# Performance work log

Hardware: AMD Instinct MI355X
Metric: run time of the kernel (lower is better)

The kernel has to match this reference:

```python
import jax, jax.numpy as jnp
import numpy as np

N = 20000        # nodes
E = 640000       # edges (avg degree 32)
IN, H1, H2 = 512, 256, 128

def setup_inputs() -> dict:
    key = jax.random.key(0)
    k_feat, k_ew, k_src, k_dst, k_w1, k_w2 = jax.random.split(key, 6)
    return {
        "features": jax.random.normal(k_feat, (N, IN), jnp.float32),
        "edge_weight": jax.random.uniform(k_ew, (E,), jnp.float32),
        "src": jax.random.randint(k_src, (E,), 0, N),
        "dst": jax.random.randint(k_dst, (E,), 0, N),
        # learned params (GraphConv weight uses xavier-style init; bias zeros)
        "W1": jax.random.normal(k_w1, (IN, H1), jnp.float32) / np.float32(np.sqrt(IN)),
        "b1": jnp.zeros((H1,), jnp.float32),
        "W2": jax.random.normal(k_w2, (H1, H2), jnp.float32) / np.float32(np.sqrt(H1)),
        "b2": jnp.zeros((H2,), jnp.float32),
    }

def reference(features, edge_weight, src, dst, W1, b1, W2, b2):
    seg = lambda v, idx: jax.ops.segment_sum(v, idx, num_segments=N)

    # --- EdgeWeightNorm(norm='both'):
    # w_e / sqrt(out_wsum(src_e) * in_wsum(dst_e))
    out_wsum = seg(edge_weight, src)           # weighted out-degree  [N]
    in_wsum = seg(edge_weight, dst)            # weighted in-degree   [N]
    nw = edge_weight * jax.lax.rsqrt(out_wsum[src]) * jax.lax.rsqrt(in_wsum[dst])  # [E]

    # --- GraphConv layer 1: norm='none', edge_weight=nw, relu
    # in_feats > out_feats -> transform first, then weighted aggregation
    h = features @ W1                          # [N, H1]
    h = seg(h[src] * nw[:, None], dst) + b1    # SpMM: sum_e nw_e * h[src_e] at dst
    h = jax.nn.relu(h)

    # --- GraphConv layer 2: norm='both' (plain degrees, clamped min 1), identity act
    ones_e = jnp.ones((E,), h.dtype)
    out_deg = jnp.maximum(seg(ones_e, src), 1.0)   # out-degrees [N]
    in_deg = jnp.maximum(seg(ones_e, dst), 1.0)    # in-degrees  [N]
    h = h * jax.lax.rsqrt(out_deg)[:, None]        # src-side norm
    h = h @ W2                                     # [N, H2] (in > out -> W first)
    h = seg(h[src], dst)                           # unweighted sum aggregation
    h = h * jax.lax.rsqrt(in_deg)[:, None] + b2    # dst-side norm + bias
    return h
```

## Files before the change

### kernel.cpp

```cpp
#include <hip/hip_runtime.h>
#include <hip/hip_bf16.h>
#include <hip/hip_fp16.h>
#include <stdint.h>

#define IN_F 512
#define H1_F 256
#define H2_F 128
#define MPAD 20096
#define NN   20000
#define NPAIR 10000
#define BH   128
#define CAP  128
#define GB1  (157 * 2)

typedef __attribute__((ext_vector_type(8))) _Float16 half8;
typedef __attribute__((ext_vector_type(4))) float f32x4;
typedef __attribute__((ext_vector_type(4))) uint32_t u32x4;

__device__ inline __half2 h2cast(uint32_t v) { return __builtin_bit_cast(__half2, v); }
__device__ inline uint32_t h2bits(__half2 v) { return __builtin_bit_cast(uint32_t, v); }

__device__ inline void gld_lds16(const uint32_t* g, uint32_t* l) {
    __builtin_amdgcn_global_load_lds((const __attribute__((address_space(1))) uint32_t*)g,
                                     (__attribute__((address_space(3))) uint32_t*)l,
                                     16, 0, 0);
}

__device__ inline uint32_t packh2(float a, float b) {
    return (uint32_t)__builtin_bit_cast(unsigned short, (_Float16)a) |
           ((uint32_t)__builtin_bit_cast(unsigned short, (_Float16)b) << 16);
}

__global__ __launch_bounds__(512) void build_and_pack(
        const int* __restrict__ dst, const int* __restrict__ src,
        const float* __restrict__ ew,
        uint32_t* __restrict__ Pd, uint32_t* __restrict__ Ps, int E, int CH,
        const float* __restrict__ W1, const float* __restrict__ W2,
        uint16_t* __restrict__ Bt1, uint16_t* __restrict__ Bt2) {
    __shared__ uint32_t pd[NN];
    __shared__ uint32_t ps[NN];
    const int b = blockIdx.x, tid = threadIdx.x;
    if (b < BH) {
        for (int i = tid; i < NN; i += 512) { pd[i] = 0; ps[i] = 0; }
        __syncthreads();
        const int e0 = b * CH, e1 = min(e0 + CH, E);
        for (int e = e0 + tid; e < e1; e += 512) {
            uint32_t v = (1u << 24) | (uint32_t)__float2uint_rn(ew[e] * 65536.0f);
            atomicAdd(&pd[dst[e]], v);
            atomicAdd(&ps[src[e]], v);
        }
        __syncthreads();
        for (int i = tid; i < NN; i += 512) {
            Pd[(size_t)b * NN + i] = pd[i];
            Ps[(size_t)b * NN + i] = ps[i];
        }
    } else {
        const int pbid = b - BH;
        const int PBLK = gridDim.x - BH;
        const int stride = PBLK * 512;
        const int t1 = IN_F * H1_F;
        const int total = t1 + H1_F * H2_F;
        for (int i = pbid * 512 + tid; i < total; i += stride) {
            if (i < t1) {
                int k = i / H1_F, n = i - k * H1_F;
                Bt1[(size_t)n * IN_F + k] =
                    __builtin_bit_cast(unsigned short, (_Float16)W1[i]);
            } else {
                int i2 = i - t1;
                int k = i2 / H2_F, n = i2 - k * H2_F;
                Bt2[(size_t)n * H1_F + k] =
                    __builtin_bit_cast(unsigned short, (_Float16)W2[i2]);
            }
        }
    }
}

__global__ __launch_bounds__(256, 1) void gemm1_and_offsets(
        const float* __restrict__ A, const uint16_t* __restrict__ Bt,
        __half* __restrict__ Cout, int M, int K,
        const uint32_t* __restrict__ Pd, const uint32_t* __restrict__ Ps,
        uint16_t* __restrict__ Od,
        int* __restrict__ in_cnt, int* __restrict__ out_cnt,
        float* __restrict__ in_rs, float* __restrict__ out_rs, int N) {
    __shared__ uint32_t Al[128 * 16];
    __shared__ uint32_t Bl[128 * 16];
    const int bx = blockIdx.x;
    const int tid = threadIdx.x;
    if (bx >= GB1) {
        int i = (bx - GB1) * 256 + tid;
        if (i >= N) return;
        uint32_t cin = 0, cout = 0, win = 0, wout = 0;
        for (int b = 0; b < BH; ++b) {
            uint32_t vd = Pd[(size_t)b * NN + i];
            Od[(size_t)b * NN + i] = (uint16_t)cin;
            cin += vd >> 24; win += vd & 0xFFFFFFu;
            uint32_t vs = Ps[(size_t)b * NN + i];
            cout += vs >> 24; wout += vs & 0xFFFFFFu;
        }
        in_cnt[i] = (int)cin;
        out_cnt[i] = (int)cout;
        in_rs[i]  = cin  ? rsqrtf((float)win  * (1.0f / 65536.0f)) : 0.f;
        out_rs[i] = cout ? rsqrtf((float)wout * (1.0f / 65536.0f)) : 0.f;
        return;
    }
    const int xg = bx % 157, yg = bx / 157;
    const int lane = tid & 63, wid = tid >> 6;
    const int wm = wid >> 1, wn = wid & 1;
    const int l15 = lane & 15, lhi = lane >> 4;
    const int brow = xg * 128, bcol = yg * 128;

    f32x4 acc[4][4];
#pragma unroll
    for (int m = 0; m < 4; ++m)
#pragma unroll
        for (int n = 0; n < 4; ++n) acc[m][n] = f32x4{0.f, 0.f, 0.f, 0.f};

    for (int k0 = 0; k0 < K; k0 += 32) {
#pragma unroll
        for (int i = 0; i < 2; ++i) {
            int g = i * 256 + tid;
            int r = g >> 2, c16 = g & 3;
            int sA = (r & 3) ^ ((r >> 2) & 3);
            int c16s = c16 ^ sA;
            int gr = min(brow + r, M - 1);
            const float* gp = A + (size_t)gr * K + k0 + c16s * 8;
            float4 fa = *(const float4*)gp;
            float4 fb = *(const float4*)(gp + 4);
            u32x4 q;
            q.x = packh2(fa.x, fa.y);
            q.y = packh2(fa.z, fa.w);
            q.z = packh2(fb.x, fb.y);
            q.w = packh2(fb.z, fb.w);
            *(u32x4*)(Al + g * 4) = q;
        }
#pragma unroll
        for (int i = 0; i < 2; ++i) {
            int chunk = i * 256 + tid;
            int r = chunk >> 2, c16 = chunk & 3;
            int c16s = c16 ^ ((r & 3) ^ ((r >> 2) & 3));
            gld_lds16((const uint32_t*)(Bt + (size_t)(bcol + r) * K + k0) + c16s * 4,
                      Bl + chunk * 4);
        }
        __syncthreads();

        half8 am[4], bm[4];
#pragma unroll
        for (int m = 0; m < 4; ++m) {
            int row = wm * 64 + m * 16 + l15;
            int sA = (row & 3) ^ ((row >> 2) & 3);
            am[m] = __builtin_bit_cast(half8,
                        *(const u32x4*)(Al + row * 16 + ((lhi ^ sA) << 2)));
        }
#pragma unroll
        for (int n = 0; n < 4; ++n) {
            int col = wn * 64 + n * 16 + l15;
            int sB = (col & 3) ^ ((col >> 2) & 3);
            bm[n] = __builtin_bit_cast(half8,
                        *(const u32x4*)(Bl + col * 16 + ((lhi ^ sB) << 2)));
        }

#pragma unroll
        for (int m = 0; m < 4; ++m)
#pragma unroll
            for (int n = 0; n < 4; ++n)
                acc[m][n] = __builtin_amdgcn_mfma_f32_16x16x32_f16(am[m], bm[n],
                                                                   acc[m][n], 0, 0, 0);
        __syncthreads();
    }

#pragma unroll
    for (int m = 0; m < 4; ++m) {
        int rbase = brow + wm * 64 + m * 16 + lhi * 4;
#pragma unroll
        for (int n = 0; n < 4; ++n) {
            int col = bcol + wn * 64 + n * 16 + l15;
#pragma unroll
            for (int j = 0; j < 4; ++j) {
                int row = rbase + j;
                if (row < M)
                    Cout[(size_t)row * H1_F + col] = __float2half(acc[m][n][j]);
            }
        }
    }
}

__global__ __launch_bounds__(512) void scatter_dst(
        const int* __restrict__ src, const int* __restrict__ dst,
        const float* __restrict__ ew,
        const uint16_t* __restrict__ Od,
        const float* __restrict__ in_rs, const float* __restrict__ out_rs,
        unsigned long long* __restrict__ s_pk, int E, int CH) {
    __shared__ uint32_t h[NPAIR];
    const int b = blockIdx.x, tid = threadIdx.x;
    for (int i = tid; i < NPAIR; i += 512) h[i] = 0;
    __syncthreads();
    const int e0 = b * CH, e1 = min(e0 + CH, E);
    const uint16_t* Ob = Od + (size_t)b * NN;
    for (int e = e0 + tid; e < e1; e += 512) {
        int d = dst[e];
        uint32_t old = atomicAdd(&h[d >> 1], 1u << ((d & 1) * 16));
        uint32_t rank = (old >> ((d & 1) * 16)) & 0xffffu;
        int s = src[e];
        float nw = ew[e] * out_rs[s] * in_rs[d];
        int p = d * CAP + (int)Ob[d] + (int)rank;
        s_pk[p] = (unsigned long long)(unsigned)s |
                  ((unsigned long long)__builtin_bit_cast(unsigned, nw) << 32);
    }
}

__global__ __launch_bounds__(256, 1) void gemm2_f16(
        const uint16_t* __restrict__ At, const uint16_t* __restrict__ Bt,
        __half* __restrict__ Cout, const int* __restrict__ rowcnt,
        int M, int Nout, int K) {
    __shared__ uint32_t Al[128 * 16];
    __shared__ uint32_t Bl[128 * 16];
    const int tid = threadIdx.x;
    const int lane = tid & 63, wid = tid >> 6;
    const int wm = wid >> 1, wn = wid & 1;
    const int l15 = lane & 15, lhi = lane >> 4;
    const int brow = blockIdx.x * 128, bcol = blockIdx.y * 128;

    f32x4 acc[4][4];
#pragma unroll
    for (int m = 0; m < 4; ++m)
#pragma unroll
        for (int n = 0; n < 4; ++n) acc[m][n] = f32x4{0.f, 0.f, 0.f, 0.f};

    for (int k0 = 0; k0 < K; k0 += 32) {
#pragma unroll
        for (int i = 0; i < 2; ++i) {
            int chunk = i * 256 + tid;
            int r = chunk >> 2, c16 = chunk & 3;
            int c16s = c16 ^ ((r & 3) ^ ((r >> 2) & 3));
            gld_lds16((const uint32_t*)(At + (size_t)(brow + r) * K + k0) + c16s * 4,
                      Al + chunk * 4);
        }
#pragma unroll
        for (int i = 0; i < 2; ++i) {
            int chunk = i * 256 + tid;
            int r = chunk >> 2, c16 = chunk & 3;
            int c16s = c16 ^ ((r & 3) ^ ((r >> 2) & 3));
            gld_lds16((const uint32_t*)(Bt + (size_t)(bcol + r) * K + k0) + c16s * 4,
                      Bl + chunk * 4);
        }
        __syncthreads();

        half8 am[4], bm[4];
#pragma unroll
        for (int m = 0; m < 4; ++m) {
            int row = wm * 64 + m * 16 + l15;
            int sA = (row & 3) ^ ((row >> 2) & 3);
            am[m] = __builtin_bit_cast(half8,
                        *(const u32x4*)(Al + row * 16 + ((lhi ^ sA) << 2)));
        }
#pragma unroll
        for (int n = 0; n < 4; ++n) {
            int col = wn * 64 + n * 16 + l15;
            int sB = (col & 3) ^ ((col >> 2) & 3);
            bm[n] = __builtin_bit_cast(half8,
                        *(const u32x4*)(Bl + col * 16 + ((lhi ^ sB) << 2)));
        }

#pragma unroll
        for (int m = 0; m < 4; ++m)
#pragma unroll
            for (int n = 0; n < 4; ++n)
                acc[m][n] = __builtin_amdgcn_mfma_f32_16x16x32_f16(am[m], bm[n],
                                                                   acc[m][n], 0, 0, 0);
        __syncthreads();
    }

#pragma unroll
    for (int m = 0; m < 4; ++m) {
        int rbase = brow + wm * 64 + m * 16 + lhi * 4;
        float scl[4];
#pragma unroll
        for (int j = 0; j < 4; ++j) {
            scl[j] = 1.f;
            if (rbase + j < M)
                scl[j] = rsqrtf(fmaxf((float)rowcnt[rbase + j], 1.f));
        }
#pragma unroll
        for (int n = 0; n < 4; ++n) {
            int col = bcol + wn * 64 + n * 16 + l15;
#pragma unroll
            for (int j = 0; j < 4; ++j) {
                int row = rbase + j;
                if (row < M)
                    Cout[(size_t)row * Nout + col] = __float2half(acc[m][n][j] * scl[j]);
            }
        }
    }
}

__global__ void spmm1_h2(const uint4* __restrict__ h4,
                         const unsigned long long* __restrict__ s_pk,
                         const int* __restrict__ in_cnt,
                         const float* __restrict__ b1, uint16_t* __restrict__ h1f, int N) {
    int bx = blockIdx.x;
    int slice = bx & 3;
    int grp = bx >> 2;
    int wid = threadIdx.x >> 6, lane = threadIdx.x & 63;
    int node = grp * 4 + wid;
    if (node >= N) return;
    int start = node * CAP, cnt = in_cnt[node];
    int s_pre = 0; uint32_t w2_pre = 0;
    if (lane < cnt) {
        unsigned long long m = s_pk[start + lane];
        s_pre = (int)(unsigned)m;
        __half hw = __float2half(__builtin_bit_cast(float, (unsigned)(m >> 32)));
        w2_pre = h2bits(__halves2half2(hw, hw));
    }
    int el = lane >> 3, fo = lane & 7;
    const uint4* hb = h4 + slice * 8 + fo;
    __half2 acc[4];
#pragma unroll
    for (int k = 0; k < 4; ++k) acc[k] = h2cast(0u);
    int cnt1 = min(cnt, 64);
    int nb = (cnt1 + 7) >> 3;
    int s[8]; uint32_t w[8]; uint4 v[8];
#pragma unroll
    for (int g = 0; g < 8; ++g) {
        if (g < nb) {
            int j = el + g * 8;
            s[g] = __shfl(s_pre, j);
            w[g] = (uint32_t)__shfl((int)w2_pre, j);
            v[g] = hb[(size_t)s[g] * 32];
        }
    }
#pragma unroll
    for (int g = 0; g < 8; ++g) {
        if (g < nb) {
            __half2 wg = h2cast(w[g]);
            acc[0] = __hfma2(wg, h2cast(v[g].x), acc[0]);
            acc[1] = __hfma2(wg, h2cast(v[g].y), acc[1]);
            acc[2] = __hfma2(wg, h2cast(v[g].z), acc[2]);
            acc[3] = __hfma2(wg, h2cast(v[g].w), acc[3]);
        }
    }
    for (int j = 64 + el; j < cnt; j += 8) {
        unsigned long long m = s_pk[start + j];
        int sx = (int)(unsigned)m;
        __half hw = __float2half(__builtin_bit_cast(float, (unsigned)(m >> 32)));
        __half2 w2h = __halves2half2(hw, hw);
        uint4 vx = hb[(size_t)sx * 32];
        acc[0] = __hfma2(w2h, h2cast(vx.x), acc[0]);
        acc[1] = __hfma2(w2h, h2cast(vx.y), acc[1]);
        acc[2] = __hfma2(w2h, h2cast(vx.z), acc[2]);
        acc[3] = __hfma2(w2h, h2cast(vx.w), acc[3]);
    }
#pragma unroll
    for (int d = 8; d < 64; d <<= 1)
#pragma unroll
        for (int k = 0; k < 4; ++k) {
            uint32_t o = (uint32_t)__shfl_xor((int)h2bits(acc[k]), d);
            acc[k] = __hadd2(acc[k], h2cast(o));
        }
    if (el == 0) {
        int fi = slice * 64 + fo * 8;
        float2 f0 = __half22float2(acc[0]);
        float2 f1 = __half22float2(acc[1]);
        float2 f2 = __half22float2(acc[2]);
        float2 f3 = __half22float2(acc[3]);
        uint4 o;
        o.x = h2bits(__halves2half2(__float2half(fmaxf(f0.x + b1[fi + 0], 0.f)),
                                    __float2half(fmaxf(f0.y + b1[fi + 1], 0.f))));
        o.y = h2bits(__halves2half2(__float2half(fmaxf(f1.x + b1[fi + 2], 0.f)),
                                    __float2half(fmaxf(f1.y + b1[fi + 3], 0.f))));
        o.z = h2bits(__halves2half2(__float2half(fmaxf(f2.x + b1[fi + 4], 0.f)),
                                    __float2half(fmaxf(f2.y + b1[fi + 5], 0.f))));
        o.w = h2bits(__halves2half2(__float2half(fmaxf(f3.x + b1[fi + 6], 0.f)),
                                    __float2half(fmaxf(f3.y + b1[fi + 7], 0.f))));
        *(uint4*)(h1f + (size_t)node * H1_F + fi) = o;
    }
}

__global__ void spmm2_h2(const uint4* __restrict__ h4,
                         const unsigned long long* __restrict__ s_pk,
                         const int* __restrict__ in_cnt,
                         const float* __restrict__ b2, float* __restrict__ out, int N) {
    const uint32_t ONE2 = 0x3C003C00u;
    int bx = blockIdx.x;
    int slice = bx & 1;
    int grp = bx >> 1;
    int wid = threadIdx.x >> 6, lane = threadIdx.x & 63;
    int node = grp * 4 + wid;
    if (node >= N) return;
    int start = node * CAP, cnt = in_cnt[node];
    int s_pre = 0;
    if (lane < cnt) s_pre = (int)(unsigned)s_pk[start + lane];
    int el = lane >> 3, fo = lane & 7;
    const uint4* hb = h4 + slice * 8 + fo;
    __half2 acc0[4], acc1[4];
#pragma unroll
    for (int k = 0; k < 4; ++k) { acc0[k] = h2cast(0u); acc1[k] = h2cast(0u); }
    int cnt1 = min(cnt, 64);
    int nb = (cnt1 + 7) >> 3;
    int s[8]; __half2 w[8]; uint4 v[8];
#pragma unroll
    for (int g = 0; g < 8; ++g) {
        if (g < nb) {
            int j = el + g * 8;
            s[g] = __shfl(s_pre, j);
            w[g] = h2cast((j < cnt1) ? ONE2 : 0u);
            v[g] = hb[(size_t)s[g] * 16];
        }
    }
#pragma unroll
    for (int g = 0; g < 4; ++g) {
        if (g < nb) {
            acc0[0] = __hfma2(w[g], h2cast(v[g].x), acc0[0]);
            acc0[1] = __hfma2(w[g], h2cast(v[g].y), acc0[1]);
            acc0[2] = __hfma2(w[g], h2cast(v[g].z), acc0[2]);
            acc0[3] = __hfma2(w[g], h2cast(v[g].w), acc0[3]);
        }
    }
#pragma unroll
    for (int g = 4; g < 8; ++g) {
        if (g < nb) {
            acc1[0] = __hfma2(w[g], h2cast(v[g].x), acc1[0]);
            acc1[1] = __hfma2(w[g], h2cast(v[g].y), acc1[1]);
            acc1[2] = __hfma2(w[g], h2cast(v[g].z), acc1[2]);
            acc1[3] = __hfma2(w[g], h2cast(v[g].w), acc1[3]);
        }
    }
    for (int j = 64 + el; j < cnt; j += 8) {
        int sx = (int)(unsigned)s_pk[start + j];
        uint4 vx = hb[(size_t)sx * 16];
        __half2 one = h2cast(ONE2);
        acc0[0] = __hfma2(one, h2cast(vx.x), acc0[0]);
        acc0[1] = __hfma2(one, h2cast(vx.y), acc0[1]);
        acc0[2] = __hfma2(one, h2cast(vx.z), acc0[2]);
        acc0[3] = __hfma2(one, h2cast(vx.w), acc0[3]);
    }
    float accf[8];
#pragma unroll
    for (int k = 0; k < 4; ++k) {
        float2 a = __half22float2(acc0[k]);
        float2 b = __half22float2(acc1[k]);
        accf[2 * k]     = a.x + b.x;
        accf[2 * k + 1] = a.y + b.y;
    }
#pragma unroll
    for (int d = 8; d < 64; d <<= 1)
#pragma unroll
        for (int k = 0; k < 8; ++k) accf[k] += __shfl_xor(accf[k], d);
    if (el == 0) {
        float rin = rsqrtf(fmaxf((float)cnt, 1.f));
        int fi = slice * 64 + fo * 8;
        f32x4 r0, r1;
        r0.x = accf[0] * rin + b2[fi + 0];
        r0.y = accf[1] * rin + b2[fi + 1];
        r0.z = accf[2] * rin + b2[fi + 2];
        r0.w = accf[3] * rin + b2[fi + 3];
        r1.x = accf[4] * rin + b2[fi + 4];
        r1.y = accf[5] * rin + b2[fi + 5];
        r1.z = accf[6] * rin + b2[fi + 6];
        r1.w = accf[7] * rin + b2[fi + 7];
        float* dp = out + (size_t)node * H2_F + fi;
        *(f32x4*)dp = r0;
        *(f32x4*)(dp + 4) = r1;
    }
}

extern "C" void kernel_launch(void* const* d_in, const int* in_sizes, int n_in,
                              void* d_out, int out_size, void* d_ws, size_t ws_size,
                              hipStream_t stream) {
    const float* features = (const float*)d_in[0];
    const float* edge_w   = (const float*)d_in[1];
    const int*   src      = (const int*)d_in[2];
    const int*   dst      = (const int*)d_in[3];
    const float* W1       = (const float*)d_in[4];
    const float* b1       = (const float*)d_in[5];
    const float* W2       = (const float*)d_in[6];
    const float* b2       = (const float*)d_in[7];
    float* out = (float*)d_out;

    const int N = in_sizes[0] / IN_F;
    const int E = in_sizes[1];
    const int CH = (E + BH - 1) / BH;

    char* base = (char*)d_ws;
    size_t off = 0;
    auto alloc = [&](size_t bytes) {
        char* p = base + off;
        off = (off + bytes + 255) & ~(size_t)255;
        return p;
    };
    int*   out_cnt   = (int*)  alloc((size_t)N * 4);
    float* out_rs    = (float*)alloc((size_t)N * 4);
    int*   in_cnt    = (int*)  alloc((size_t)N * 4);
    float* in_rs     = (float*)alloc((size_t)N * 4);
    unsigned long long* s_pk = (unsigned long long*)alloc((size_t)NN * CAP * 8);
    uint16_t* Bt1    = (uint16_t*)alloc((size_t)H1_F * IN_F * 2);
    uint16_t* Bt2    = (uint16_t*)alloc((size_t)H2_F * H1_F * 2);
    __half* h_f16    = (__half*)alloc((size_t)MPAD * H1_F * 2);
    uint32_t* big    = (uint32_t*)alloc((size_t)BH * NN * 4 * 2 + (size_t)BH * NN * 2);
    uint32_t* Pd = big;
    uint32_t* Ps = big + (size_t)BH * NN;
    uint16_t* Od = (uint16_t*)(Ps + (size_t)BH * NN);
    uint16_t* h1f = (uint16_t*)big;
    __half*   h2f = (__half*)((uint16_t*)big + (size_t)MPAD * H1_F);
    (void)ws_size;

    build_and_pack<<<256, 512, 0, stream>>>(dst, src, edge_w, Pd, Ps, E, CH,
                                            W1, W2, Bt1, Bt2);

    int goBlocks = GB1 + (N + 255) / 256;
    gemm1_and_offsets<<<goBlocks, 256, 0, stream>>>(features, Bt1, h_f16, N, IN_F,
                                                    Pd, Ps, Od, in_cnt, out_cnt,
                                                    in_rs, out_rs, N);

    scatter_dst<<<BH, 512, 0, stream>>>(src, dst, edge_w, Od,
                                        in_rs, out_rs, s_pk, E, CH);

    int grp = (N + 3) / 4;
    spmm1_h2<<<grp * 4, 256, 0, stream>>>((const uint4*)h_f16, s_pk,
                                          in_cnt, b1, h1f, N);
    dim3 g2(MPAD / 128, 1);
    gemm2_f16<<<g2, 256, 0, stream>>>(h1f, Bt2, h2f, out_cnt, N, H2_F, H1_F);
    spmm2_h2<<<grp * 2, 256, 0, stream>>>((const uint4*)h2f, s_pk,
                                          in_cnt, b2, out, N);
}
```

Before: 122.7 us.

## Co-schedule GEMM1 with edge scatter and share A tile across column halves

The per-node offsets/rsqrt computation moves out of the GEMM1 launch into its own small kernel. The edge scatter then runs as extra blocks inside the GEMM1 launch instead of as a separate kernel. GEMM1 now uses 512-thread blocks, where each block converts one 128-row A tile to fp16 once and two 256-thread halves compute both 128-column output halves. This halves the fp32 feature reads and conversions, and lets the scatter overlap with the GEMM. The cost is a larger LDS footprint and bigger blocks, which may lower occupancy, and the scatter blocks now compete with GEMM blocks for CUs.

```diff
diff --git a/kernel.cpp b/kernel.cpp
--- a/kernel.cpp
+++ b/kernel.cpp
@@ -11,7 +11,7 @@
 #define NPAIR 10000
 #define BH   128
 #define CAP  128
-#define GB1  (157 * 2)
+#define GT1  157
 
 typedef __attribute__((ext_vector_type(8))) _Float16 half8;
 typedef __attribute__((ext_vector_type(4))) float f32x4;
@@ -75,39 +75,65 @@
     }
 }
 
-__global__ __launch_bounds__(256, 1) void gemm1_and_offsets(
+__global__ void offsets_kernel(const uint32_t* __restrict__ Pd,
+                               const uint32_t* __restrict__ Ps,
+                               uint16_t* __restrict__ Od,
+                               int* __restrict__ in_cnt, int* __restrict__ out_cnt,
+                               float* __restrict__ in_rs, float* __restrict__ out_rs, int N) {
+    int i = blockIdx.x * blockDim.x + threadIdx.x;
+    if (i >= N) return;
+    uint32_t cin = 0, cout = 0, win = 0, wout = 0;
+    for (int b = 0; b < BH; ++b) {
+        uint32_t vd = Pd[(size_t)b * NN + i];
+        Od[(size_t)b * NN + i] = (uint16_t)cin;
+        cin += vd >> 24; win += vd & 0xFFFFFFu;
+        uint32_t vs = Ps[(size_t)b * NN + i];
+        cout += vs >> 24; wout += vs & 0xFFFFFFu;
+    }
+    in_cnt[i] = (int)cin;
+    out_cnt[i] = (int)cout;
+    in_rs[i]  = cin  ? rsqrtf((float)win  * (1.0f / 65536.0f)) : 0.f;
+    out_rs[i] = cout ? rsqrtf((float)wout * (1.0f / 65536.0f)) : 0.f;
+}
+
+__global__ __launch_bounds__(512, 1) void gemm1_and_scatter(
         const float* __restrict__ A, const uint16_t* __restrict__ Bt,
         __half* __restrict__ Cout, int M, int K,
-        const uint32_t* __restrict__ Pd, const uint32_t* __restrict__ Ps,
-        uint16_t* __restrict__ Od,
-        int* __restrict__ in_cnt, int* __restrict__ out_cnt,
-        float* __restrict__ in_rs, float* __restrict__ out_rs, int N) {
-    __shared__ uint32_t Al[128 * 16];
-    __shared__ uint32_t Bl[128 * 16];
-    const int bx = blockIdx.x;
-    const int tid = threadIdx.x;
-    if (bx >= GB1) {
-        int i = (bx - GB1) * 256 + tid;
-        if (i >= N) return;
-        uint32_t cin = 0, cout = 0, win = 0, wout = 0;
-        for (int b = 0; b < BH; ++b) {
-            uint32_t vd = Pd[(size_t)b * NN + i];
-            Od[(size_t)b * NN + i] = (uint16_t)cin;
-            cin += vd >> 24; win += vd & 0xFFFFFFu;
-            uint32_t vs = Ps[(size_t)b * NN + i];
-            cout += vs >> 24; wout += vs & 0xFFFFFFu;
-        }
-        in_cnt[i] = (int)cin;
-        out_cnt[i] = (int)cout;
-        in_rs[i]  = cin  ? rsqrtf((float)win  * (1.0f / 65536.0f)) : 0.f;
-        out_rs[i] = cout ? rsqrtf((float)wout * (1.0f / 65536.0f)) : 0.f;
+        const int* __restrict__ src, const int* __restrict__ dst,
+        const float* __restrict__ ew, const uint16_t* __restrict__ Od,
+        const float* __restrict__ in_rs, const float* __restrict__ out_rs,
+        unsigned long long* __restrict__ s_pk, int E, int CH) {
+    __shared__ uint32_t smem[NPAIR];
+    const int bx = blockIdx.x, tid = threadIdx.x;
+
+    if (bx >= GT1) {
+        uint32_t* h = smem;
+        const int b = bx - GT1;
+        for (int i = tid; i < NPAIR; i += 512) h[i] = 0;
+        __syncthreads();
+        const int e0 = b * CH, e1 = min(e0 + CH, E);
+        const uint16_t* Ob = Od + (size_t)b * NN;
+        for (int e = e0 + tid; e < e1; e += 512) {
+            int d = dst[e];
+            uint32_t old = atomicAdd(&h[d >> 1], 1u << ((d & 1) * 16));
+            uint32_t rank = (old >> ((d & 1) * 16)) & 0xffffu;
+            int s = src[e];
+            float nw = ew[e] * out_rs[s] * in_rs[d];
+            int p = d * CAP + (int)Ob[d] + (int)rank;
+            s_pk[p] = (unsigned long long)(unsigned)s |
+                      ((unsigned long long)__builtin_bit_cast(unsigned, nw) << 32);
+        }
         return;
     }
-    const int xg = bx % 157, yg = bx / 157;
-    const int lane = tid & 63, wid = tid >> 6;
-    const int wm = wid >> 1, wn = wid & 1;
+
+    uint32_t* Al = smem;
+    const int cg = tid >> 8;
+    const int tid2 = tid & 255;
+    uint32_t* Bl = smem + 2048 + cg * 2048;
+    const int lane = tid2 & 63, wid2 = tid2 >> 6;
+    const int wm = wid2 >> 1, wn = wid2 & 1;
     const int l15 = lane & 15, lhi = lane >> 4;
-    const int brow = xg * 128, bcol = yg * 128;
+    const int brow = bx * 128, bcol = cg * 128;
 
     f32x4 acc[4][4];
 #pragma unroll
@@ -116,9 +142,8 @@
         for (int n = 0; n < 4; ++n) acc[m][n] = f32x4{0.f, 0.f, 0.f, 0.f};
 
     for (int k0 = 0; k0 < K; k0 += 32) {
-#pragma unroll
-        for (int i = 0; i < 2; ++i) {
-            int g = i * 256 + tid;
+        {
+            int g = tid;
             int r = g >> 2, c16 = g & 3;
             int sA = (r & 3) ^ ((r >> 2) & 3);
             int c16s = c16 ^ sA;
@@ -135,7 +160,7 @@
         }
 #pragma unroll
         for (int i = 0; i < 2; ++i) {
-            int chunk = i * 256 + tid;
+            int chunk = i * 256 + tid2;
             int r = chunk >> 2, c16 = chunk & 3;
             int c16s = c16 ^ ((r & 3) ^ ((r >> 2) & 3));
             gld_lds16((const uint32_t*)(Bt + (size_t)(bcol + r) * K + k0) + c16s * 4,
@@ -181,30 +206,6 @@
                     Cout[(size_t)row * H1_F + col] = __float2half(acc[m][n][j]);
             }
         }
-    }
-}
-
-__global__ __launch_bounds__(512) void scatter_dst(
-        const int* __restrict__ src, const int* __restrict__ dst,
-        const float* __restrict__ ew,
-        const uint16_t* __restrict__ Od,
-        const float* __restrict__ in_rs, const float* __restrict__ out_rs,
-        unsigned long long* __restrict__ s_pk, int E, int CH) {
-    __shared__ uint32_t h[NPAIR];
-    const int b = blockIdx.x, tid = threadIdx.x;
-    for (int i = tid; i < NPAIR; i += 512) h[i] = 0;
-    __syncthreads();
-    const int e0 = b * CH, e1 = min(e0 + CH, E);
-    const uint16_t* Ob = Od + (size_t)b * NN;
-    for (int e = e0 + tid; e < e1; e += 512) {
-        int d = dst[e];
-        uint32_t old = atomicAdd(&h[d >> 1], 1u << ((d & 1) * 16));
-        uint32_t rank = (old >> ((d & 1) * 16)) & 0xffffu;
-        int s = src[e];
-        float nw = ew[e] * out_rs[s] * in_rs[d];
-        int p = d * CAP + (int)Ob[d] + (int)rank;
-        s_pk[p] = (unsigned long long)(unsigned)s |
-                  ((unsigned long long)__builtin_bit_cast(unsigned, nw) << 32);
     }
 }
 
@@ -506,13 +507,12 @@
     build_and_pack<<<256, 512, 0, stream>>>(dst, src, edge_w, Pd, Ps, E, CH,
                                             W1, W2, Bt1, Bt2);
 
-    int goBlocks = GB1 + (N + 255) / 256;
-    gemm1_and_offsets<<<goBlocks, 256, 0, stream>>>(features, Bt1, h_f16, N, IN_F,
-                                                    Pd, Ps, Od, in_cnt, out_cnt,
-                                                    in_rs, out_rs, N);
-
-    scatter_dst<<<BH, 512, 0, stream>>>(src, dst, edge_w, Od,
-                                        in_rs, out_rs, s_pk, E, CH);
+    offsets_kernel<<<(N + 255) / 256, 256, 0, stream>>>(Pd, Ps, Od, in_cnt, out_cnt,
+                                                        in_rs, out_rs, N);
+
+    gemm1_and_scatter<<<GT1 + BH, 512, 0, stream>>>(features, Bt1, h_f16, N, IN_F,
+                                                    src, dst, edge_w, Od,
+                                                    in_rs, out_rs, s_pk, E, CH);
 
     int grp = (N + 3) / 4;
     spmm1_h2<<<grp * 4, 256, 0, stream>>>((const uint4*)h_f16, s_pk,
```

New measurement: 129.3 us. +5.4%, slower.
